# Performance work log

Measured on AMD Instinct MI355X. Metric: run time of the kernel, lower is better.

Reference implementation:

```python
import jax, jax.numpy as jnp
import numpy as np
import math

N_HEADS = 16
N_POINTS = 4
EPS = 1e-6


def layer_norm(x, g, b):
    m = x.mean(-1, keepdims=True)
    v = ((x - m) ** 2).mean(-1, keepdims=True)
    return (x - m) / jnp.sqrt(v + EPS) * g + b


def ref_points(H, W, dtype):
    # matches CrossSelfAtt.get_reference_points for one square level -> (1, H*W, 1, 2) in (x, y)
    ys = (jnp.arange(H, dtype=dtype) + 0.5) / H
    xs = (jnp.arange(W, dtype=dtype) + 0.5) / W
    gy, gx = jnp.meshgrid(ys, xs, indexing='ij')
    return jnp.stack([gx.reshape(-1), gy.reshape(-1)], -1)[None, :, None, :]


def bilinear(v, H, W, loc):
    # v: (B, H*W, nH, Dh); loc: (B, Lq, nH, P, 2) normalized [0,1]; zero padding, align_corners=False
    B, _, nH, Dh = v.shape
    Lq, P = loc.shape[1], loc.shape[3]
    x = loc[..., 0] * W - 0.5
    y = loc[..., 1] * H - 0.5
    x0 = jnp.floor(x)
    y0 = jnp.floor(y)
    wx1 = x - x0
    wy1 = y - y0
    x0i = x0.astype(jnp.int32)
    y0i = y0.astype(jnp.int32)
    vt = v.transpose(0, 2, 1, 3)  # (B, nH, HW, Dh)

    def corner(xi, yi, w):
        valid = (xi >= 0) & (xi < W) & (yi >= 0) & (yi < H)
        idx = jnp.clip(yi, 0, H - 1) * W + jnp.clip(xi, 0, W - 1)  # (B, Lq, nH, P)
        idx_t = idx.transpose(0, 2, 1, 3).reshape(B, nH, Lq * P)
        g = jnp.take_along_axis(vt, idx_t[..., None], axis=2).reshape(B, nH, Lq, P, Dh)
        return g.transpose(0, 2, 1, 3, 4) * (w * valid)[..., None]

    return (corner(x0i, y0i, (1 - wx1) * (1 - wy1))
            + corner(x0i + 1, y0i, wx1 * (1 - wy1))
            + corner(x0i, y0i + 1, (1 - wx1) * wy1)
            + corner(x0i + 1, y0i + 1, wx1 * wy1))


def msda(query, value_in, shapes, ref, Wv, bv, Woff, boff, Wa, ba, Wo, bo):
    # standard Deformable-DETR MSDeformAttn forward
    B, Lq, D = query.shape
    nH, P, L = N_HEADS, N_POINTS, len(shapes)
    Dh = D // nH
    value = (value_in @ Wv + bv).reshape(B, -1, nH, Dh)
    off = (query @ Woff + boff).reshape(B, Lq, nH, L, P, 2)
    aw = jax.nn.softmax((query @ Wa + ba).reshape(B, Lq, nH, L * P), -1).reshape(B, Lq, nH, L, P)
    norm = jnp.asarray([[w_, h_] for (h_, w_) in shapes], dtype=query.dtype)  # (L, 2) = (W, H)
    loc = ref[:, :, None, :, None, :] + off / norm[None, None, None, :, None, :]
    out = jnp.zeros((B, Lq, nH, Dh), query.dtype)
    start = 0
    for l, (H_, W_) in enumerate(shapes):
        samp = bilinear(value[:, start:start + H_ * W_], H_, W_, loc[:, :, :, l])
        out = out + (samp * aw[:, :, :, l, :, None]).sum(3)
        start += H_ * W_
    return out.reshape(B, Lq, D) @ Wo + bo


def setup_inputs() -> dict:
    key = jax.random.key(0)
    B, Lq, Lf, D = 2, 4096, 4096, 768
    nH, P, L = N_HEADS, N_POINTS, 1
    ks = jax.random.split(key, 20)
    w = lambda k, s: jax.random.normal(k, s, jnp.float32) * 0.02
    return {
        'query': jax.random.normal(ks[0], (B, Lq, D), jnp.float32),
        'feat': jax.random.normal(ks[1], (B, Lf, D), jnp.float32),
        'spatial_shapes': jnp.array([[64, 64]], jnp.int32),
        'level_start_index': jnp.array([0], jnp.int32),
        'qn_W': w(ks[2], (D, D)), 'qn_b': jnp.zeros((D,)), 'qn_g': jnp.ones((D,)), 'qn_beta': jnp.zeros((D,)),
        'fn_W': w(ks[3], (D, D)), 'fn_b': jnp.zeros((D,)), 'fn_g': jnp.ones((D,)), 'fn_beta': jnp.zeros((D,)),
        'nm_g': jnp.ones((D,)), 'nm_beta': jnp.zeros((D,)),
        'gamma1': jax.random.normal(ks[4], (D,), jnp.float32) * 0.1,
        'c_Wv': w(ks[5], (D, D)), 'c_bv': jnp.zeros((D,)),
        'c_Woff': w(ks[6], (D, nH * L * P * 2)),
        'c_boff': jax.random.uniform(ks[7], (nH * L * P * 2,), jnp.float32, -3.0, 3.0),
        'c_Wa': w(ks[8], (D, nH * L * P)), 'c_ba': jnp.zeros((nH * L * P,)),
        'c_Wo': w(ks[9], (D, D)), 'c_bo': jnp.zeros((D,)),
        's_Wv': w(ks[10], (D, D)), 's_bv': jnp.zeros((D,)),
        's_Woff': w(ks[11], (D, nH * L * P * 2)),
        's_boff': jax.random.uniform(ks[12], (nH * L * P * 2,), jnp.float32, -3.0, 3.0),
        's_Wa': w(ks[13], (D, nH * L * P)), 's_ba': jnp.zeros((nH * L * P,)),
        's_Wo': w(ks[14], (D, D)), 's_bo': jnp.zeros((D,)),
    }


def reference(query, feat, spatial_shapes, level_start_index, qn_W, qn_b, qn_g, qn_beta, fn_W, fn_b, fn_g, fn_beta, nm_g, nm_beta, gamma1, c_Wv, c_bv, c_Woff, c_boff, c_Wa, c_ba, c_Wo, c_bo, s_Wv, s_bv, s_Woff, s_boff, s_Wa, s_ba, s_Wo, s_bo):
    shapes = [(int(h), int(w_)) for h, w_ in np.asarray(spatial_shapes)]
    qe = int(math.sqrt(query.shape[1]))
    ref = ref_points(qe, qe, query.dtype)  # (1, Lq, 1, 2)
    qn = layer_norm(query @ qn_W + qn_b, qn_g, qn_beta)
    fn = layer_norm(feat @ fn_W + fn_b, fn_g, fn_beta)
    attn = msda(qn, fn, shapes, ref, c_Wv, c_bv, c_Woff, c_boff, c_Wa, c_ba, c_Wo, c_bo)
    attn1 = layer_norm(attn, nm_g, nm_beta)
    attn2 = msda(attn1, attn1, [(qe, qe)], ref, s_Wv, s_bv, s_Woff, s_boff, s_Wa, s_ba, s_Wo, s_bo)
    # note: source uses gamma1 for BOTH terms (gamma2 is unused)
    return attn * gamma1 + attn2 * gamma1
```

## Files before the change

### kernel.cpp

```cpp
#include <hip/hip_runtime.h>
#include <hip/hip_bf16.h>
#include <math.h>

#define D_MODEL 768
#define NH 16
#define DH 48
#define NP 4
#define LQ 4096
#define BB 2
#define MTOT (BB * LQ)

typedef __attribute__((ext_vector_type(8))) _Float16 half8_t;
typedef __attribute__((ext_vector_type(4))) float floatx4;

__device__ __forceinline__ void load_lds16(const void* g, void* l) {
    __builtin_amdgcn_global_load_lds((const __attribute__((address_space(1))) void*)g,
                                     (__attribute__((address_space(3))) void*)l, 16, 0, 0);
}

template <int MODE>
__device__ __forceinline__ void gemm_body(
    const _Float16* __restrict__ A, const _Float16* __restrict__ Wt,
    const float* __restrict__ bias, float* __restrict__ C, int ldc,
    int tm, int tn,
    const float* __restrict__ attn, const float* __restrict__ gamma)
{
    constexpr int K = 768;
    __shared__ _Float16 As[128 * 32];
    __shared__ _Float16 Bs[128 * 32];

    const int bm = tm * 128, bn = tn * 128;
    const int t = threadIdx.x;
    const int lane = t & 63;
    const int w = t >> 6;
    const int wm = (w >> 1) * 64, wn = (w & 1) * 64;

    floatx4 acc[4][4] = {};

    const int r0 = t >> 2;
    const int c8 = (t & 3) * 8;
    _Float16* AsW0 = &As[w * 512];
    _Float16* AsW1 = &As[2048 + w * 512];
    _Float16* BsW0 = &Bs[w * 512];
    _Float16* BsW1 = &Bs[2048 + w * 512];

    const int lrow = lane & 15;
    const int lk = (lane >> 4) * 8;

    for (int kt = 0; kt < K; kt += 32) {
        load_lds16(A + (size_t)(bm + r0) * K + kt + c8, AsW0);
        load_lds16(A + (size_t)(bm + 64 + r0) * K + kt + c8, AsW1);
        load_lds16(Wt + (size_t)(bn + r0) * K + kt + c8, BsW0);
        load_lds16(Wt + (size_t)(bn + 64 + r0) * K + kt + c8, BsW1);
        __syncthreads();

        half8_t af[4], bf[4];
#pragma unroll
        for (int i = 0; i < 4; ++i) {
            af[i] = *(const half8_t*)&As[(wm + i * 16 + lrow) * 32 + lk];
            bf[i] = *(const half8_t*)&Bs[(wn + i * 16 + lrow) * 32 + lk];
        }
#pragma unroll
        for (int i = 0; i < 4; ++i)
#pragma unroll
            for (int j = 0; j < 4; ++j)
                acc[i][j] = __builtin_amdgcn_mfma_f32_16x16x32_f16(af[i], bf[j], acc[i][j], 0, 0, 0);
        __syncthreads();
    }

    const int rquad = (lane >> 4) * 4;
#pragma unroll
    for (int i = 0; i < 4; ++i) {
#pragma unroll
        for (int j = 0; j < 4; ++j) {
            const int col = bn + wn + j * 16 + lrow;
            const float bcol = bias[col];
#pragma unroll
            for (int r = 0; r < 4; ++r) {
                const size_t row = (size_t)(bm + wm + i * 16 + rquad + r);
                float v = acc[i][j][r] + bcol;
                if (MODE == 1) v = (attn[row * ldc + col] + v) * gamma[col];
                C[row * (size_t)ldc + col] = v;
            }
        }
    }
}

template <int MODE>
__global__ __launch_bounds__(256) void gemm_mfma(
    const _Float16* __restrict__ A, const _Float16* __restrict__ Wt,
    const float* __restrict__ bias, float* __restrict__ C,
    const float* __restrict__ attn, const float* __restrict__ gamma)
{
    const int bid = blockIdx.x;
    const int swz = (bid & 7) * 48 + (bid >> 3);
    gemm_body<MODE>(A, Wt, bias, C, 768, swz & 63, swz >> 6, attn, gamma);
}

__global__ __launch_bounds__(256) void dual_gemm(
    const _Float16* __restrict__ A0, const _Float16* __restrict__ W0,
    const float* __restrict__ b0, float* __restrict__ C0, int ldc0, int cnt0,
    const _Float16* __restrict__ A1, const _Float16* __restrict__ W1,
    const float* __restrict__ b1, float* __restrict__ C1, int ldc1, int cnt1)
{
    int bid = blockIdx.x;
    const _Float16 *A, *Wt; const float* bias; float* C; int ldc, cnt;
    if (bid < cnt0) { A = A0; Wt = W0; bias = b0; C = C0; ldc = ldc0; cnt = cnt0; }
    else { bid -= cnt0; A = A1; Wt = W1; bias = b1; C = C1; ldc = ldc1; cnt = cnt1; }
    const int q = cnt >> 3;
    const int swz = (bid & 7) * q + (bid >> 3);
    gemm_body<0>(A, Wt, bias, C, ldc, swz & 63, swz >> 6, nullptr, nullptr);
}

__device__ __forceinline__ void ln_body(
    const float* __restrict__ X, _Float16* __restrict__ A,
    const float* __restrict__ g, const float* __restrict__ beta, int row)
{
    const float* x = X + (size_t)row * D_MODEL;
    const int t = threadIdx.x;
    float v0 = x[t], v1 = x[t + 256], v2 = x[t + 512];
    float s = v0 + v1 + v2;
    float s2 = v0 * v0 + v1 * v1 + v2 * v2;
#pragma unroll
    for (int m = 1; m < 64; m <<= 1) {
        s += __shfl_xor(s, m);
        s2 += __shfl_xor(s2, m);
    }
    __shared__ float red[8];
    const int wave = t >> 6, lane = t & 63;
    if (lane == 0) { red[wave] = s; red[wave + 4] = s2; }
    __syncthreads();
    s = red[0] + red[1] + red[2] + red[3];
    s2 = red[4] + red[5] + red[6] + red[7];
    const float mean = s * (1.f / 768.f);
    const float var = s2 * (1.f / 768.f) - mean * mean;
    const float rstd = rsqrtf(var + 1e-6f);
    _Float16* arow = A + (size_t)row * D_MODEL;
    arow[t]       = (_Float16)((v0 - mean) * rstd * g[t] + beta[t]);
    arow[t + 256] = (_Float16)((v1 - mean) * rstd * g[t + 256] + beta[t + 256]);
    arow[t + 512] = (_Float16)((v2 - mean) * rstd * g[t + 512] + beta[t + 512]);
}

__global__ __launch_bounds__(256) void ln2_emit(
    const float* __restrict__ X0, _Float16* __restrict__ A0,
    const float* __restrict__ g0, const float* __restrict__ b0,
    const float* __restrict__ X1, _Float16* __restrict__ A1,
    const float* __restrict__ g1, const float* __restrict__ b1)
{
    const int row = blockIdx.x;
    if (row < MTOT) ln_body(X0, A0, g0, b0, row);
    else            ln_body(X1, A1, g1, b1, row - MTOT);
}

__global__ __launch_bounds__(256) void ln_emit(
    const float* __restrict__ X, _Float16* __restrict__ A,
    const float* __restrict__ g, const float* __restrict__ beta)
{
    ln_body(X, A, g, beta, blockIdx.x);
}

__global__ __launch_bounds__(256) void convert_act2(
    const float* __restrict__ X0, _Float16* __restrict__ D0,
    const float* __restrict__ X1, _Float16* __restrict__ D1)
{
    const int i = blockIdx.x * 256 + threadIdx.x;
    const int sel = i / (MTOT * 192);
    const int r = i - sel * (MTOT * 192);
    const float* X = sel ? X1 : X0;
    _Float16* D = sel ? D1 : D0;
    const int c4 = r * 4;
    const float4 v = *(const float4*)(X + (size_t)c4);
    _Float16 o[4] = {(_Float16)v.x, (_Float16)v.y, (_Float16)v.z, (_Float16)v.w};
    *(uint2*)(D + (size_t)c4) = *(uint2*)o;
}

__global__ __launch_bounds__(256) void convert_w6(
    const float* __restrict__ w0, const float* __restrict__ w1,
    const float* __restrict__ w2, const float* __restrict__ w3,
    const float* __restrict__ w4, const float* __restrict__ w5,
    _Float16* __restrict__ Wall)
{
    const int wi = blockIdx.y;
    const float* W = (wi == 0) ? w0 : (wi == 1) ? w1 : (wi == 2) ? w2
                   : (wi == 3) ? w3 : (wi == 4) ? w4 : w5;
    _Float16* Wt = Wall + (size_t)wi * 768 * 768;

    __shared__ float tile[32][33];
    const int tk0 = (blockIdx.x / 24) * 32;
    const int tn0 = (blockIdx.x % 24) * 32;
    const int t = threadIdx.x;
#pragma unroll
    for (int r = 0; r < 4; ++r) {
        const int row = r * 8 + (t >> 5);
        const int col = t & 31;
        tile[row][col] = W[(size_t)(tk0 + row) * 768 + tn0 + col];
    }
    __syncthreads();
    const int n = t >> 3;
    const int kq = (t & 7) * 4;
    _Float16* dst = Wt + (size_t)(tn0 + n) * 768 + tk0 + kq;
#pragma unroll
    for (int u = 0; u < 4; ++u) dst[u] = (_Float16)tile[kq + u][n];
}

__global__ __launch_bounds__(256) void convert_offa(
    const float* __restrict__ Woff_c, const float* __restrict__ Wa_c,
    const float* __restrict__ boff_c, const float* __restrict__ ba_c,
    const float* __restrict__ Woff_s, const float* __restrict__ Wa_s,
    const float* __restrict__ boff_s, const float* __restrict__ ba_s,
    _Float16* __restrict__ Wc, _Float16* __restrict__ Ws,
    float* __restrict__ bias_c, float* __restrict__ bias_s)
{
    const int i = blockIdx.x * 256 + threadIdx.x;
    if (i >= 2 * 256 * 192) return;
    const int pair = i / (256 * 192);
    const int r = i - pair * (256 * 192);
    const int n = r / 192;
    const int k0 = (r - n * 192) * 4;
    const float* Woff = pair ? Woff_s : Woff_c;
    const float* Wa = pair ? Wa_s : Wa_c;
    _Float16* dst = pair ? Ws : Wc;
    _Float16* row = dst + (size_t)n * 768;
#pragma unroll
    for (int u = 0; u < 4; ++u) {
        const int k = k0 + u;
        float v = (n < 128) ? Woff[(size_t)k * 128 + n]
                : (n < 192) ? Wa[(size_t)k * 64 + (n - 128)] : 0.f;
        row[k] = (_Float16)v;
    }
    if (k0 == 0) {
        const float* boff = pair ? boff_s : boff_c;
        const float* ba = pair ? ba_s : ba_c;
        float* bias = pair ? bias_s : bias_c;
        bias[n] = (n < 128) ? boff[n] : (n < 192) ? ba[n - 128] : 0.f;
    }
}

__global__ __launch_bounds__(256) void offaw_post(
    const float* __restrict__ offc,
    float* __restrict__ loc, float* __restrict__ aw)
{
    const int i = blockIdx.x * 256 + threadIdx.x;
    if (i >= MTOT * NH) return;
    const int h = i & (NH - 1);
    const int bq = i >> 4;
    const int q = bq & (LQ - 1);

    const float* orow = offc + (size_t)bq * 256 + h * 8;
    const float* arow = offc + (size_t)bq * 256 + 128 + h * 4;

    float a0 = arow[0], a1 = arow[1], a2 = arow[2], a3 = arow[3];
    float mx = fmaxf(fmaxf(a0, a1), fmaxf(a2, a3));
    float e0 = expf(a0 - mx), e1 = expf(a1 - mx), e2 = expf(a2 - mx), e3 = expf(a3 - mx);
    float r = 1.f / (e0 + e1 + e2 + e3);

    const float refx = ((q & 63) + 0.5f) * (1.f / 64.f);
    const float refy = ((q >> 6) + 0.5f) * (1.f / 64.f);
#pragma unroll
    for (int p = 0; p < 4; ++p) {
        loc[(size_t)i * 8 + p * 2 + 0] = refx + orow[p * 2 + 0] * (1.f / 64.f);
        loc[(size_t)i * 8 + p * 2 + 1] = refy + orow[p * 2 + 1] * (1.f / 64.f);
    }
    aw[(size_t)i * 4 + 0] = e0 * r;
    aw[(size_t)i * 4 + 1] = e1 * r;
    aw[(size_t)i * 4 + 2] = e2 * r;
    aw[(size_t)i * 4 + 3] = e3 * r;
}

__global__ __launch_bounds__(256) void sample_f4(
    const float* __restrict__ value, const float* __restrict__ loc,
    const float* __restrict__ aw, _Float16* __restrict__ A)
{
    const int idx = blockIdx.x * 256 + threadIdx.x;
    const int bqh = idx / 12;
    const int c = idx - bqh * 12;
    const int d0 = c * 4;
    const int h = bqh & (NH - 1);
    const int bq = bqh >> 4;
    const int b = bq >> 12;

    const float4 l01 = *(const float4*)(loc + (size_t)bqh * 8);
    const float4 l23 = *(const float4*)(loc + (size_t)bqh * 8 + 4);
    const float4 w4 = *(const float4*)(aw + (size_t)bqh * 4);
    const float lx[4] = {l01.x, l01.z, l23.x, l23.z};
    const float ly[4] = {l01.y, l01.w, l23.y, l23.w};
    const float wp4[4] = {w4.x, w4.y, w4.z, w4.w};

    const float* vbase = value + (size_t)b * LQ * D_MODEL + h * DH + d0;

    float4 acc = {0.f, 0.f, 0.f, 0.f};
#pragma unroll
    for (int p = 0; p < 4; ++p) {
        const float x = lx[p] * 64.f - 0.5f;
        const float y = ly[p] * 64.f - 0.5f;
        const float xf = floorf(x), yf = floorf(y);
        const float wx1 = x - xf, wy1 = y - yf;
        const float wx0 = 1.f - wx1, wy0 = 1.f - wy1;
        const int x0 = (int)xf, y0 = (int)yf;
        const int x1 = x0 + 1, y1 = y0 + 1;
        const float wp = wp4[p];
        const bool vx0 = (x0 >= 0) && (x0 < 64);
        const bool vx1 = (x1 >= 0) && (x1 < 64);
        const bool vy0 = (y0 >= 0) && (y0 < 64);
        const bool vy1 = (y1 >= 0) && (y1 < 64);
        const float cw[4] = {wp * wx0 * wy0, wp * wx1 * wy0, wp * wx0 * wy1, wp * wx1 * wy1};
        const bool cv[4] = {vx0 && vy0, vx1 && vy0, vx0 && vy1, vx1 && vy1};
        const int cxy[4][2] = {{x0, y0}, {x1, y0}, {x0, y1}, {x1, y1}};
#pragma unroll
        for (int k = 0; k < 4; ++k) {
            if (cv[k]) {
                const float4 g = *(const float4*)(vbase + (size_t)(cxy[k][1] * 64 + cxy[k][0]) * D_MODEL);
                acc.x += cw[k] * g.x; acc.y += cw[k] * g.y;
                acc.z += cw[k] * g.z; acc.w += cw[k] * g.w;
            }
        }
    }

    _Float16* arow = A + (size_t)bq * D_MODEL + h * DH + d0;
    _Float16 o[4] = {(_Float16)acc.x, (_Float16)acc.y, (_Float16)acc.z, (_Float16)acc.w};
    *(uint2*)arow = *(uint2*)o;
}

extern "C" void kernel_launch(void* const* d_in, const int* in_sizes, int n_in,
                              void* d_out, int out_size, void* d_ws, size_t ws_size,
                              hipStream_t stream)
{
    const float* query   = (const float*)d_in[0];
    const float* feat    = (const float*)d_in[1];
    const float* qn_W    = (const float*)d_in[4];
    const float* qn_b    = (const float*)d_in[5];
    const float* qn_g    = (const float*)d_in[6];
    const float* qn_beta = (const float*)d_in[7];
    const float* fn_W    = (const float*)d_in[8];
    const float* fn_b    = (const float*)d_in[9];
    const float* fn_g    = (const float*)d_in[10];
    const float* fn_beta = (const float*)d_in[11];
    const float* nm_g    = (const float*)d_in[12];
    const float* nm_beta = (const float*)d_in[13];
    const float* gamma1  = (const float*)d_in[14];
    const float* c_Wv    = (const float*)d_in[15];
    const float* c_bv    = (const float*)d_in[16];
    const float* c_Woff  = (const float*)d_in[17];
    const float* c_boff  = (const float*)d_in[18];
    const float* c_Wa    = (const float*)d_in[19];
    const float* c_ba    = (const float*)d_in[20];
    const float* c_Wo    = (const float*)d_in[21];
    const float* c_bo    = (const float*)d_in[22];
    const float* s_Wv    = (const float*)d_in[23];
    const float* s_bv    = (const float*)d_in[24];
    const float* s_Woff  = (const float*)d_in[25];
    const float* s_boff  = (const float*)d_in[26];
    const float* s_Wa    = (const float*)d_in[27];
    const float* s_ba    = (const float*)d_in[28];
    const float* s_Wo    = (const float*)d_in[29];
    const float* s_bo    = (const float*)d_in[30];

    float* ws = (float*)d_ws;
    const size_t SZ = (size_t)MTOT * D_MODEL;
    float* buf0 = ws;
    float* buf1 = ws + SZ;
    float* buf2 = ws + 2 * SZ;
    float* buf3 = ws + 3 * SZ;
    _Float16* slotA = (_Float16*)(ws + 4 * SZ);
    _Float16* slotB = (_Float16*)(ws + 4 * SZ + SZ / 2);
    float* loc    = ws + 5 * SZ;
    float* aws    = loc + (size_t)MTOT * 128;
    float* bias_c = aws + (size_t)MTOT * 64;
    float* bias_s = bias_c + 256;
    _Float16* W6 = (_Float16*)(bias_s + 256);
    _Float16* W_qn  = W6 + (size_t)0 * 768 * 768;
    _Float16* W_fn  = W6 + (size_t)1 * 768 * 768;
    _Float16* W_cWv = W6 + (size_t)2 * 768 * 768;
    _Float16* W_cWo = W6 + (size_t)3 * 768 * 768;
    _Float16* W_sWv = W6 + (size_t)4 * 768 * 768;
    _Float16* W_sWo = W6 + (size_t)5 * 768 * 768;
    _Float16* Woffa_c = W6 + (size_t)6 * 768 * 768;
    _Float16* Woffa_s = Woffa_c + (size_t)256 * 768;

    float* out = (float*)d_out;
    const dim3 blk(256);

    convert_w6<<<dim3(576, 6), blk, 0, stream>>>(qn_W, fn_W, c_Wv, c_Wo, s_Wv, s_Wo, W6);
    convert_offa<<<384, blk, 0, stream>>>(c_Woff, c_Wa, c_boff, c_ba,
                                          s_Woff, s_Wa, s_boff, s_ba,
                                          Woffa_c, Woffa_s, bias_c, bias_s);
    convert_act2<<<12288, blk, 0, stream>>>(query, slotA, feat, slotB);

    dual_gemm<<<768, blk, 0, stream>>>(slotA, W_qn, qn_b, buf0, 768, 384,
                                       slotB, W_fn, fn_b, buf1, 768, 384);
    ln2_emit<<<2 * MTOT, blk, 0, stream>>>(buf0, slotA, qn_g, qn_beta,
                                           buf1, slotB, fn_g, fn_beta);
    dual_gemm<<<512, blk, 0, stream>>>(slotB, W_cWv, c_bv, buf2, 768, 384,
                                       slotA, Woffa_c, bias_c, buf0, 256, 128);
    offaw_post<<<(MTOT * NH + 255) / 256, blk, 0, stream>>>(buf0, loc, aws);
    sample_f4<<<MTOT * NH * 12 / 256, blk, 0, stream>>>(buf2, loc, aws, slotB);
    gemm_mfma<0><<<384, blk, 0, stream>>>(slotB, W_cWo, c_bo, buf3, nullptr, nullptr);

    ln_emit<<<MTOT, blk, 0, stream>>>(buf3, slotA, nm_g, nm_beta);
    dual_gemm<<<512, blk, 0, stream>>>(slotA, W_sWv, s_bv, buf2, 768, 384,
                                       slotA, Woffa_s, bias_s, buf0, 256, 128);
    offaw_post<<<(MTOT * NH + 255) / 256, blk, 0, stream>>>(buf0, loc, aws);
    sample_f4<<<MTOT * NH * 12 / 256, blk, 0, stream>>>(buf2, loc, aws, slotB);
    gemm_mfma<1><<<384, blk, 0, stream>>>(slotB, W_sWo, s_bo, out, buf3, gamma1);
}
```

Measured before the change: 400.0 us.

## Double-buffer GEMM LDS tiles, use wave-per-row layernorm, swizzle sampler blocks

The MFMA GEMM body now keeps two LDS buffers and issues the next k-tile's global-to-LDS loads before computing on the current one, leaving one barrier per iteration instead of two. LayerNorm kernels now give each 64-lane wave a full row, dropping the shared-memory cross-wave reduction and its barrier, with four rows per block. The deformable sampling kernel gets a block-index swizzle meant to improve cache locality across concurrently running blocks. Double-buffering doubles LDS use per block, which may lower occupancy. The swizzle hardcodes 768 and assumes the grid size is a multiple of 8.

```diff
diff --git a/kernel.cpp b/kernel.cpp
--- a/kernel.cpp
+++ b/kernel.cpp
@@ -26,8 +26,9 @@
     const float* __restrict__ attn, const float* __restrict__ gamma)
 {
     constexpr int K = 768;
-    __shared__ _Float16 As[128 * 32];
-    __shared__ _Float16 Bs[128 * 32];
+    constexpr int NT = K / 32;
+    __shared__ _Float16 As[2][128 * 32];
+    __shared__ _Float16 Bs[2][128 * 32];
 
     const int bm = tm * 128, bn = tn * 128;
     const int t = threadIdx.x;
@@ -39,33 +40,46 @@
 
     const int r0 = t >> 2;
     const int c8 = (t & 3) * 8;
-    _Float16* AsW0 = &As[w * 512];
-    _Float16* AsW1 = &As[2048 + w * 512];
-    _Float16* BsW0 = &Bs[w * 512];
-    _Float16* BsW1 = &Bs[2048 + w * 512];
+    const size_t arow0 = (size_t)(bm + r0) * K + c8;
+    const size_t arow1 = (size_t)(bm + 64 + r0) * K + c8;
+    const size_t brow0 = (size_t)(bn + r0) * K + c8;
+    const size_t brow1 = (size_t)(bn + 64 + r0) * K + c8;
 
     const int lrow = lane & 15;
     const int lk = (lane >> 4) * 8;
 
-    for (int kt = 0; kt < K; kt += 32) {
-        load_lds16(A + (size_t)(bm + r0) * K + kt + c8, AsW0);
-        load_lds16(A + (size_t)(bm + 64 + r0) * K + kt + c8, AsW1);
-        load_lds16(Wt + (size_t)(bn + r0) * K + kt + c8, BsW0);
-        load_lds16(Wt + (size_t)(bn + 64 + r0) * K + kt + c8, BsW1);
-        __syncthreads();
-
+    load_lds16(A + arow0, &As[0][w * 512]);
+    load_lds16(A + arow1, &As[0][2048 + w * 512]);
+    load_lds16(Wt + brow0, &Bs[0][w * 512]);
+    load_lds16(Wt + brow1, &Bs[0][2048 + w * 512]);
+    __syncthreads();
+
+    for (int ti = 0; ti < NT; ++ti) {
+        const int cur = ti & 1;
+        if (ti + 1 < NT) {
+            const int kn = (ti + 1) * 32;
+            const int nxt = cur ^ 1;
+            load_lds16(A + arow0 + kn, &As[nxt][w * 512]);
+            load_lds16(A + arow1 + kn, &As[nxt][2048 + w * 512]);
+            load_lds16(Wt + brow0 + kn, &Bs[nxt][w * 512]);
+            load_lds16(Wt + brow1 + kn, &Bs[nxt][2048 + w * 512]);
+        }
+
+        const _Float16* Ac = As[cur];
+        const _Float16* Bc = Bs[cur];
         half8_t af[4], bf[4];
 #pragma unroll
         for (int i = 0; i < 4; ++i) {
-            af[i] = *(const half8_t*)&As[(wm + i * 16 + lrow) * 32 + lk];
-            bf[i] = *(const half8_t*)&Bs[(wn + i * 16 + lrow) * 32 + lk];
+            af[i] = *(const half8_t*)&Ac[(wm + i * 16 + lrow) * 32 + lk];
+            bf[i] = *(const half8_t*)&Bc[(wn + i * 16 + lrow) * 32 + lk];
         }
 #pragma unroll
         for (int i = 0; i < 4; ++i)
 #pragma unroll
             for (int j = 0; j < 4; ++j)
                 acc[i][j] = __builtin_amdgcn_mfma_f32_16x16x32_f16(af[i], bf[j], acc[i][j], 0, 0, 0);
-        __syncthreads();
+
+        if (ti + 1 < NT) __syncthreads();
     }
 
     const int rquad = (lane >> 4) * 4;
@@ -112,51 +126,53 @@
     gemm_body<0>(A, Wt, bias, C, ldc, swz & 63, swz >> 6, nullptr, nullptr);
 }
 
-__device__ __forceinline__ void ln_body(
+__device__ __forceinline__ void ln_wave_body(
     const float* __restrict__ X, _Float16* __restrict__ A,
     const float* __restrict__ g, const float* __restrict__ beta, int row)
 {
+    const int lane = threadIdx.x & 63;
     const float* x = X + (size_t)row * D_MODEL;
-    const int t = threadIdx.x;
-    float v0 = x[t], v1 = x[t + 256], v2 = x[t + 512];
-    float s = v0 + v1 + v2;
-    float s2 = v0 * v0 + v1 * v1 + v2 * v2;
+    float v[12];
+    float s = 0.f, s2 = 0.f;
+#pragma unroll
+    for (int j = 0; j < 12; ++j) {
+        v[j] = x[lane + 64 * j];
+        s += v[j];
+        s2 += v[j] * v[j];
+    }
 #pragma unroll
     for (int m = 1; m < 64; m <<= 1) {
         s += __shfl_xor(s, m);
         s2 += __shfl_xor(s2, m);
     }
-    __shared__ float red[8];
-    const int wave = t >> 6, lane = t & 63;
-    if (lane == 0) { red[wave] = s; red[wave + 4] = s2; }
-    __syncthreads();
-    s = red[0] + red[1] + red[2] + red[3];
-    s2 = red[4] + red[5] + red[6] + red[7];
     const float mean = s * (1.f / 768.f);
     const float var = s2 * (1.f / 768.f) - mean * mean;
     const float rstd = rsqrtf(var + 1e-6f);
     _Float16* arow = A + (size_t)row * D_MODEL;
-    arow[t]       = (_Float16)((v0 - mean) * rstd * g[t] + beta[t]);
-    arow[t + 256] = (_Float16)((v1 - mean) * rstd * g[t + 256] + beta[t + 256]);
-    arow[t + 512] = (_Float16)((v2 - mean) * rstd * g[t + 512] + beta[t + 512]);
-}
-
-__global__ __launch_bounds__(256) void ln2_emit(
+#pragma unroll
+    for (int j = 0; j < 12; ++j) {
+        const int cc = lane + 64 * j;
+        arow[cc] = (_Float16)((v[j] - mean) * rstd * g[cc] + beta[cc]);
+    }
+}
+
+__global__ __launch_bounds__(256) void ln2_wave(
     const float* __restrict__ X0, _Float16* __restrict__ A0,
     const float* __restrict__ g0, const float* __restrict__ b0,
     const float* __restrict__ X1, _Float16* __restrict__ A1,
     const float* __restrict__ g1, const float* __restrict__ b1)
 {
-    const int row = blockIdx.x;
-    if (row < MTOT) ln_body(X0, A0, g0, b0, row);
-    else            ln_body(X1, A1, g1, b1, row - MTOT);
-}
-
-__global__ __launch_bounds__(256) void ln_emit(
+    const int r = blockIdx.x * 4 + (threadIdx.x >> 6);
+    if (r < MTOT) ln_wave_body(X0, A0, g0, b0, r);
+    else          ln_wave_body(X1, A1, g1, b1, r - MTOT);
+}
+
+__global__ __launch_bounds__(256) void ln_wave(
     const float* __restrict__ X, _Float16* __restrict__ A,
     const float* __restrict__ g, const float* __restrict__ beta)
 {
-    ln_body(X, A, g, beta, blockIdx.x);
+    const int r = blockIdx.x * 4 + (threadIdx.x >> 6);
+    ln_wave_body(X, A, g, beta, r);
 }
 
 __global__ __launch_bounds__(256) void convert_act2(
@@ -271,7 +287,9 @@
     const float* __restrict__ value, const float* __restrict__ loc,
     const float* __restrict__ aw, _Float16* __restrict__ A)
 {
-    const int idx = blockIdx.x * 256 + threadIdx.x;
+    const int bid = blockIdx.x;
+    const int swz = (bid & 7) * 768 + (bid >> 3);
+    const int idx = swz * 256 + threadIdx.x;
     const int bqh = idx / 12;
     const int c = idx - bqh * 12;
     const int d0 = c * 4;
@@ -388,15 +406,15 @@
 
     dual_gemm<<<768, blk, 0, stream>>>(slotA, W_qn, qn_b, buf0, 768, 384,
                                        slotB, W_fn, fn_b, buf1, 768, 384);
-    ln2_emit<<<2 * MTOT, blk, 0, stream>>>(buf0, slotA, qn_g, qn_beta,
-                                           buf1, slotB, fn_g, fn_beta);
+    ln2_wave<<<2 * MTOT / 4, blk, 0, stream>>>(buf0, slotA, qn_g, qn_beta,
+                                               buf1, slotB, fn_g, fn_beta);
     dual_gemm<<<512, blk, 0, stream>>>(slotB, W_cWv, c_bv, buf2, 768, 384,
                                        slotA, Woffa_c, bias_c, buf0, 256, 128);
     offaw_post<<<(MTOT * NH + 255) / 256, blk, 0, stream>>>(buf0, loc, aws);
     sample_f4<<<MTOT * NH * 12 / 256, blk, 0, stream>>>(buf2, loc, aws, slotB);
     gemm_mfma<0><<<384, blk, 0, stream>>>(slotB, W_cWo, c_bo, buf3, nullptr, nullptr);
 
-    ln_emit<<<MTOT, blk, 0, stream>>>(buf3, slotA, nm_g, nm_beta);
+    ln_wave<<<MTOT / 4, blk, 0, stream>>>(buf3, slotA, nm_g, nm_beta);
     dual_gemm<<<512, blk, 0, stream>>>(slotA, W_sWv, s_bv, buf2, 768, 384,
                                        slotA, Woffa_s, bias_s, buf0, 256, 128);
     offaw_post<<<(MTOT * NH + 255) / 256, blk, 0, stream>>>(buf0, loc, aws);
```

Result: faster. 382.4 us (-4.4%).
